# Performance work log

Measured on AMD Instinct MI355X. Metric: run time of the kernel, lower is better.

## Reference

```python
import jax, jax.numpy as jnp
from jax import lax
import numpy as np

B, S, H, DIN, BIN, NH, NL = 32, 256, 256, 16, 2, 8, 3
DH = H // NH


def setup_inputs() -> dict:
    key = jax.random.key(0)
    it = iter(jax.random.split(key, 40))
    def nrm(shape, s=0.05):
        return jax.random.normal(next(it), shape, jnp.float32) * s
    return {
        "parts": jax.random.normal(next(it), (B, S, DIN), jnp.float32),
        "bin_info": jax.random.normal(next(it), (B, BIN), jnp.float32),
        "target": jax.random.randint(next(it), (B, S), 0, S, dtype=jnp.int32),
        "pe_W1": nrm((H // 2, DIN)), "pe_b1": jnp.zeros((H // 2,), jnp.float32),
        "pe_W2": nrm((H // 2, H // 2)), "pe_b2": jnp.zeros((H // 2,), jnp.float32),
        "be_W1": nrm((H // 4, BIN)), "be_b1": jnp.zeros((H // 4,), jnp.float32),
        "be_W2": nrm((H // 4, H // 4)), "be_b2": jnp.zeros((H // 4,), jnp.float32),
        "pos_emb": nrm((S, H // 4)),
        "tr_Wqkv": nrm((NL, 3 * H, H)), "tr_bqkv": jnp.zeros((NL, 3 * H), jnp.float32),
        "tr_Wo": nrm((NL, H, H)), "tr_bo": jnp.zeros((NL, H), jnp.float32),
        "tr_ln1_g": jnp.ones((NL, H), jnp.float32), "tr_ln1_b": jnp.zeros((NL, H), jnp.float32),
        "tr_ff_W1": nrm((NL, 2 * H, H)), "tr_ff_b1": jnp.zeros((NL, 2 * H), jnp.float32),
        "tr_ff_W2": nrm((NL, H, 2 * H)), "tr_ff_b2": jnp.zeros((NL, H), jnp.float32),
        "tr_ln2_g": jnp.ones((NL, H), jnp.float32), "tr_ln2_b": jnp.zeros((NL, H), jnp.float32),
        "lstm_Wih": nrm((4 * H, H)), "lstm_Whh": nrm((4 * H, H)),
        "lstm_bih": jnp.zeros((4 * H,), jnp.float32), "lstm_bhh": jnp.zeros((4 * H,), jnp.float32),
        "ptr_W": nrm((H, H)), "ptr_b": jnp.zeros((H,), jnp.float32),
        "ptr_v": nrm((H,)),
    }


def _ln(x, g, b):
    m = x.mean(-1, keepdims=True)
    v = ((x - m) ** 2).mean(-1, keepdims=True)
    return (x - m) / jnp.sqrt(v + 1e-5) * g + b


def _forward(parts, bin_info, target, pe_W1, pe_b1, pe_W2, pe_b2,
             be_W1, be_b1, be_W2, be_b2, pos_emb,
             tr_Wqkv, tr_bqkv, tr_Wo, tr_bo, tr_ln1_g, tr_ln1_b,
             tr_ff_W1, tr_ff_b1, tr_ff_W2, tr_ff_b2, tr_ln2_g, tr_ln2_b,
             lstm_Wih, lstm_Whh, lstm_bih, lstm_bhh, ptr_W, ptr_b, ptr_v):
    # --- encode_inputs (dropout inactive in eval) ---
    p = jax.nn.relu(parts @ pe_W1.T + pe_b1) @ pe_W2.T + pe_b2            # [B,S,H/2]
    bb = jax.nn.relu(bin_info @ be_W1.T + be_b1) @ be_W2.T + be_b2        # [B,H/4]
    bb = jnp.broadcast_to(bb[:, None, :], (B, S, H // 4))
    pe = jnp.broadcast_to(pos_emb[None], (B, S, H // 4))
    x = jnp.concatenate([p, bb, pe], axis=-1)                             # [B,S,H]
    scale = 1.0 / np.sqrt(DH)
    for l in range(NL):  # post-norm TransformerEncoderLayer, relu FFN
        qkv = x @ tr_Wqkv[l].T + tr_bqkv[l]
        q, k, v = jnp.split(qkv, 3, axis=-1)
        q = q.reshape(B, S, NH, DH).transpose(0, 2, 1, 3)
        k = k.reshape(B, S, NH, DH).transpose(0, 2, 1, 3)
        v = v.reshape(B, S, NH, DH).transpose(0, 2, 1, 3)
        a = jax.nn.softmax(jnp.einsum('bhqd,bhkd->bhqk', q, k) * scale, axis=-1)
        o = jnp.einsum('bhqk,bhkd->bhqd', a, v).transpose(0, 2, 1, 3).reshape(B, S, H)
        x = _ln(x + o @ tr_Wo[l].T + tr_bo[l], tr_ln1_g[l], tr_ln1_b[l])
        ff = jax.nn.relu(x @ tr_ff_W1[l].T + tr_ff_b1[l]) @ tr_ff_W2[l].T + tr_ff_b2[l]
        x = _ln(x + ff, tr_ln2_g[l], tr_ln2_b[l])
    enc = x
    # Note: the original's inner MultiheadAttention calls never feed the
    # returned step_logits (part_logit is overwritten), so the faithful output is
    # logits[b,t,i] = v . tanh(ptr(h_t) + ptr(enc_i)), vectorized over i here.
    e_proj = enc @ ptr_W.T + ptr_b                                        # [B,S,H]
    bidx = jnp.arange(B)

    def step(carry, tgt_t):
        h, c, xin = carry
        g = xin @ lstm_Wih.T + lstm_bih + h @ lstm_Whh.T + lstm_bhh
        i, f, gg, o = jnp.split(g, 4, axis=-1)
        c = jax.nn.sigmoid(f) * c + jax.nn.sigmoid(i) * jnp.tanh(gg)
        h = jax.nn.sigmoid(o) * jnp.tanh(c)
        hp = h @ ptr_W.T + ptr_b                                          # [B,H]
        logits = jnp.tanh(hp[:, None, :] + e_proj) @ ptr_v                # [B,S]
        nxt = enc[bidx, tgt_t]                                            # teacher forcing
        return (h, c, nxt), logits

    z = jnp.zeros((B, H), jnp.float32)
    _, logits = lax.scan(step, (z, z, z), target.T)                       # [S,B,S]
    return logits.transpose(1, 0, 2)                                      # [B,S,S]


def reference(parts, bin_info, target, pe_W1, pe_b1, pe_W2, pe_b2,
              be_W1, be_b1, be_W2, be_b2, pos_emb,
              tr_Wqkv, tr_bqkv, tr_Wo, tr_bo, tr_ln1_g, tr_ln1_b,
              tr_ff_W1, tr_ff_b1, tr_ff_W2, tr_ff_b2, tr_ln2_g, tr_ln2_b,
              lstm_Wih, lstm_Whh, lstm_bih, lstm_bhh, ptr_W, ptr_b, ptr_v):
    return _forward(parts, bin_info, target, pe_W1, pe_b1, pe_W2, pe_b2,
                    be_W1, be_b1, be_W2, be_b2, pos_emb,
                    tr_Wqkv, tr_bqkv, tr_Wo, tr_bo, tr_ln1_g, tr_ln1_b,
                    tr_ff_W1, tr_ff_b1, tr_ff_W2, tr_ff_b2, tr_ln2_g, tr_ln2_b,
                    lstm_Wih, lstm_Whh, lstm_bih, lstm_bhh, ptr_W, ptr_b, ptr_v)
```

## Files before the change

kernel.cpp:

```cpp
#include <hip/hip_runtime.h>
#include <cstddef>

#define DEV __device__ __forceinline__

DEV float fexp2(float x) { return __builtin_amdgcn_exp2f(x); }
DEV float frcp(float x)  { return __builtin_amdgcn_rcpf(x); }
DEV float fsigm(float x) { return frcp(1.0f + fexp2(-1.44269504f * x)); }
DEV float ftanh_(float x){ return 1.0f - 2.0f * frcp(1.0f + fexp2(2.88539008f * x)); }

typedef _Float16 h2t __attribute__((ext_vector_type(2)));
typedef _Float16 v8h __attribute__((ext_vector_type(8)));
typedef float v4f __attribute__((ext_vector_type(4)));
union U32H2 { unsigned int u; h2t h; };
DEV h2t u2h(unsigned int u) { U32H2 x; x.u = u; return x.h; }

template <int BM, int BN, bool RELU, bool OUTF16>
__global__ __launch_bounds__(256) void hgemm_kernel(
    const _Float16* __restrict__ A, const _Float16* __restrict__ W,
    const float* __restrict__ bias1, const float* __restrict__ bias2,
    void* __restrict__ Cout, int M, int N, int K)
{
    constexpr int MT = BM / 32;
    constexpr int NT = BN / 32;
    constexpr int RA = BM / 64;
    constexpr int RB = BN / 64;
    __shared__ _Float16 As[BM * 32];
    __shared__ _Float16 Bs[BN * 32];

    const int tid = threadIdx.x;
    const int lane = tid & 63;
    const int lm = lane & 15, lq = lane >> 4;
    const int wrow = ((tid >> 6) & 1) * (BM / 2);
    const int wcol = (tid >> 7) * (BN / 2);
    const int m0 = blockIdx.x * BM, n0 = blockIdx.y * BN;
    const _Float16* Ab = A + (size_t)m0 * K;
    const _Float16* Wb = W + (size_t)n0 * K;

    v4f acc[MT][NT];
#pragma unroll
    for (int i = 0; i < MT; ++i)
#pragma unroll
        for (int j = 0; j < NT; ++j) acc[i][j] = (v4f){0.f, 0.f, 0.f, 0.f};

    const int rowS = tid >> 2, qS = tid & 3;

    uint4 ra[RA], rb[RB];
#pragma unroll
    for (int r = 0; r < RA; ++r)
        ra[r] = *(const uint4*)(Ab + (size_t)(rowS + 64 * r) * K + qS * 8);
#pragma unroll
    for (int r = 0; r < RB; ++r)
        rb[r] = *(const uint4*)(Wb + (size_t)(rowS + 64 * r) * K + qS * 8);

    for (int k0 = 0; k0 < K; k0 += 32) {
        __syncthreads();
#pragma unroll
        for (int r = 0; r < RA; ++r)
            *(uint4*)(As + (size_t)(tid + 256 * r) * 8) = ra[r];
#pragma unroll
        for (int r = 0; r < RB; ++r)
            *(uint4*)(Bs + (size_t)(tid + 256 * r) * 8) = rb[r];
        __syncthreads();
        int kn = k0 + 32;
        if (kn < K) {
#pragma unroll
            for (int r = 0; r < RA; ++r)
                ra[r] = *(const uint4*)(Ab + (size_t)(rowS + 64 * r) * K + kn + qS * 8);
#pragma unroll
            for (int r = 0; r < RB; ++r)
                rb[r] = *(const uint4*)(Wb + (size_t)(rowS + 64 * r) * K + kn + qS * 8);
        }
        v8h af[MT], bf[NT];
#pragma unroll
        for (int i = 0; i < MT; ++i)
            af[i] = *(const v8h*)(As + (size_t)(wrow + i * 16 + lm) * 32 + lq * 8);
#pragma unroll
        for (int j = 0; j < NT; ++j)
            bf[j] = *(const v8h*)(Bs + (size_t)(wcol + j * 16 + lm) * 32 + lq * 8);
#pragma unroll
        for (int i = 0; i < MT; ++i)
#pragma unroll
            for (int j = 0; j < NT; ++j)
                acc[i][j] = __builtin_amdgcn_mfma_f32_16x16x32_f16(
                    af[i], bf[j], acc[i][j], 0, 0, 0);
    }

#pragma unroll
    for (int j = 0; j < NT; ++j) {
        int col = n0 + wcol + j * 16 + lm;
        float bv = bias1[col];
        if (bias2) bv += bias2[col];
#pragma unroll
        for (int i = 0; i < MT; ++i) {
            int rbase = m0 + wrow + i * 16 + lq * 4;
#pragma unroll
            for (int rg = 0; rg < 4; ++rg) {
                float vv = acc[i][j][rg] + bv;
                if (RELU) vv = fmaxf(vv, 0.f);
                if (OUTF16)
                    ((_Float16*)Cout)[(size_t)(rbase + rg) * N + col] = (_Float16)vv;
                else
                    ((float*)Cout)[(size_t)(rbase + rg) * N + col] = vv;
            }
        }
    }
}

__global__ __launch_bounds__(256) void hgemm_gather_kernel(
    const _Float16* __restrict__ X16, const int* __restrict__ target,
    const _Float16* __restrict__ W, const float* __restrict__ bias1,
    _Float16* __restrict__ Cout, int N, int K)
{
    constexpr int BM = 64, BN = 128, MT = 2, NT = 4, RB = 2;
    __shared__ _Float16 As[BM * 32];
    __shared__ _Float16 Bs[BN * 32];

    const int tid = threadIdx.x;
    const int lane = tid & 63;
    const int lm = lane & 15, lq = lane >> 4;
    const int wrow = ((tid >> 6) & 1) * (BM / 2);
    const int wcol = (tid >> 7) * (BN / 2);
    const int m0 = blockIdx.x * BM, n0 = blockIdx.y * BN;
    const _Float16* Wb = W + (size_t)n0 * K;

    v4f acc[MT][NT];
#pragma unroll
    for (int i = 0; i < MT; ++i)
#pragma unroll
        for (int j = 0; j < NT; ++j) acc[i][j] = (v4f){0.f, 0.f, 0.f, 0.f};

    const int rowS = tid >> 2, qS = tid & 3;

    const int m = m0 + rowS;
    const int bb = m >> 8, tt = m & 255;
    const bool valid = (tt > 0);
    const _Float16* arow = X16;
    if (valid) {
        int src = target[bb * 256 + tt - 1];
        arow = X16 + ((size_t)(bb * 256 + src)) * 256;
    }

    uint4 ra, rb[RB];
    ra = valid ? *(const uint4*)(arow + qS * 8) : (uint4){0u, 0u, 0u, 0u};
#pragma unroll
    for (int r = 0; r < RB; ++r)
        rb[r] = *(const uint4*)(Wb + (size_t)(rowS + 64 * r) * K + qS * 8);

    for (int k0 = 0; k0 < K; k0 += 32) {
        __syncthreads();
        *(uint4*)(As + (size_t)tid * 8) = ra;
#pragma unroll
        for (int r = 0; r < RB; ++r)
            *(uint4*)(Bs + (size_t)(tid + 256 * r) * 8) = rb[r];
        __syncthreads();
        int kn = k0 + 32;
        if (kn < K) {
            ra = valid ? *(const uint4*)(arow + kn + qS * 8)
                       : (uint4){0u, 0u, 0u, 0u};
#pragma unroll
            for (int r = 0; r < RB; ++r)
                rb[r] = *(const uint4*)(Wb + (size_t)(rowS + 64 * r) * K + kn + qS * 8);
        }
        v8h af[MT], bf[NT];
#pragma unroll
        for (int i = 0; i < MT; ++i)
            af[i] = *(const v8h*)(As + (size_t)(wrow + i * 16 + lm) * 32 + lq * 8);
#pragma unroll
        for (int j = 0; j < NT; ++j)
            bf[j] = *(const v8h*)(Bs + (size_t)(wcol + j * 16 + lm) * 32 + lq * 8);
#pragma unroll
        for (int i = 0; i < MT; ++i)
#pragma unroll
            for (int j = 0; j < NT; ++j)
                acc[i][j] = __builtin_amdgcn_mfma_f32_16x16x32_f16(
                    af[i], bf[j], acc[i][j], 0, 0, 0);
    }

#pragma unroll
    for (int j = 0; j < NT; ++j) {
        int col = n0 + wcol + j * 16 + lm;
        float bv = bias1[col];
#pragma unroll
        for (int i = 0; i < MT; ++i) {
            int rbase = m0 + wrow + i * 16 + lq * 4;
#pragma unroll
            for (int rg = 0; rg < 4; ++rg)
                Cout[(size_t)(rbase + rg) * N + col] =
                    (_Float16)(acc[i][j][rg] + bv);
        }
    }
}

__global__ __launch_bounds__(256) void hgemm_ln_kernel(
    const _Float16* __restrict__ A, const _Float16* __restrict__ W,
    const float* __restrict__ bias, const float* __restrict__ gamma,
    const float* __restrict__ beta, float* __restrict__ X,
    _Float16* __restrict__ X16, int K)
{
    constexpr int BM = 64, BN = 256, MT = 2, NT = 8, RA = 1, RB = 4;
    __shared__ _Float16 As[BM * 32];
    __shared__ _Float16 Bs[BN * 32];
    __shared__ float redS[2][BM][2];

    const int tid = threadIdx.x;
    const int lane = tid & 63;
    const int lm = lane & 15, lq = lane >> 4;
    const int wrow = ((tid >> 6) & 1) * 32;
    const int wcol = (tid >> 7) * 128;
    const int half = tid >> 7;
    const int m0 = blockIdx.x * BM;
    const _Float16* Ab = A + (size_t)m0 * K;

    v4f acc[MT][NT];
#pragma unroll
    for (int i = 0; i < MT; ++i)
#pragma unroll
        for (int j = 0; j < NT; ++j) acc[i][j] = (v4f){0.f, 0.f, 0.f, 0.f};

    const int rowS = tid >> 2, qS = tid & 3;

    uint4 ra[RA], rb[RB];
#pragma unroll
    for (int r = 0; r < RA; ++r)
        ra[r] = *(const uint4*)(Ab + (size_t)(rowS + 64 * r) * K + qS * 8);
#pragma unroll
    for (int r = 0; r < RB; ++r)
        rb[r] = *(const uint4*)(W + (size_t)(rowS + 64 * r) * K + qS * 8);

    for (int k0 = 0; k0 < K; k0 += 32) {
        __syncthreads();
#pragma unroll
        for (int r = 0; r < RA; ++r)
            *(uint4*)(As + (size_t)(tid + 256 * r) * 8) = ra[r];
#pragma unroll
        for (int r = 0; r < RB; ++r)
            *(uint4*)(Bs + (size_t)(tid + 256 * r) * 8) = rb[r];
        __syncthreads();
        int kn = k0 + 32;
        if (kn < K) {
#pragma unroll
            for (int r = 0; r < RA; ++r)
                ra[r] = *(const uint4*)(Ab + (size_t)(rowS + 64 * r) * K + kn + qS * 8);
#pragma unroll
            for (int r = 0; r < RB; ++r)
                rb[r] = *(const uint4*)(W + (size_t)(rowS + 64 * r) * K + kn + qS * 8);
        }
        v8h af[MT], bf[NT];
#pragma unroll
        for (int i = 0; i < MT; ++i)
            af[i] = *(const v8h*)(As + (size_t)(wrow + i * 16 + lm) * 32 + lq * 8);
#pragma unroll
        for (int j = 0; j < NT; ++j)
            bf[j] = *(const v8h*)(Bs + (size_t)(wcol + j * 16 + lm) * 32 + lq * 8);
#pragma unroll
        for (int i = 0; i < MT; ++i)
#pragma unroll
            for (int j = 0; j < NT; ++j)
                acc[i][j] = __builtin_amdgcn_mfma_f32_16x16x32_f16(
                    af[i], bf[j], acc[i][j], 0, 0, 0);
    }

    float s[MT][4], s2[MT][4];
#pragma unroll
    for (int i = 0; i < MT; ++i)
#pragma unroll
        for (int rg = 0; rg < 4; ++rg) { s[i][rg] = 0.f; s2[i][rg] = 0.f; }
#pragma unroll
    for (int j = 0; j < NT; ++j) {
        int col = wcol + j * 16 + lm;
        float bv = bias[col];
#pragma unroll
        for (int i = 0; i < MT; ++i) {
            int rbase = m0 + wrow + i * 16 + lq * 4;
#pragma unroll
            for (int rg = 0; rg < 4; ++rg) {
                float y = acc[i][j][rg] + bv + X[(size_t)(rbase + rg) * 256 + col];
                acc[i][j][rg] = y;
                s[i][rg] += y;
                s2[i][rg] += y * y;
            }
        }
    }
#pragma unroll
    for (int i = 0; i < MT; ++i)
#pragma unroll
        for (int rg = 0; rg < 4; ++rg) {
            float a = s[i][rg], b2 = s2[i][rg];
#pragma unroll
            for (int m = 1; m < 16; m <<= 1) {
                a += __shfl_xor(a, m);
                b2 += __shfl_xor(b2, m);
            }
            if (lm == 0) {
                int rloc = wrow + i * 16 + lq * 4 + rg;
                redS[half][rloc][0] = a;
                redS[half][rloc][1] = b2;
            }
        }
    __syncthreads();
#pragma unroll
    for (int i = 0; i < MT; ++i) {
#pragma unroll
        for (int rg = 0; rg < 4; ++rg) {
            int rloc = wrow + i * 16 + lq * 4 + rg;
            float st = redS[0][rloc][0] + redS[1][rloc][0];
            float s2t = redS[0][rloc][1] + redS[1][rloc][1];
            float mean = st * (1.f / 256.f);
            float var = s2t * (1.f / 256.f) - mean * mean;
            float inv = rsqrtf(var + 1e-5f);
            size_t rowb = (size_t)(m0 + rloc) * 256;
#pragma unroll
            for (int j = 0; j < NT; ++j) {
                int col = wcol + j * 16 + lm;
                float o = (acc[i][j][rg] - mean) * inv * gamma[col] + beta[col];
                X[rowb + col] = o;
                X16[rowb + col] = (_Float16)o;
            }
        }
    }
}

__global__ __launch_bounds__(256) void cvt_fused_kernel(
    const float* __restrict__ s0, const float* __restrict__ s1,
    const float* __restrict__ s2, const float* __restrict__ s3,
    const float* __restrict__ s4, const float* __restrict__ s5,
    _Float16* __restrict__ dst,
    const float* __restrict__ Whh, unsigned int* __restrict__ WB,
    const float* __restrict__ bih, const float* __restrict__ bhh,
    float* __restrict__ PB)
{
    if (blockIdx.x < 7424) {
        int i = blockIdx.x * 256 + threadIdx.x;
        if (i >= 1900544) return;
        float val;
        if (i < 589824)       val = s0[i];
        else if (i < 786432)  val = s1[i - 589824];
        else if (i < 1179648) val = s2[i - 786432];
        else if (i < 1572864) val = s3[i - 1179648];
        else if (i < 1835008) {
            int idx = i - 1572864;
            int rp = idx >> 8, k = idx & 255;
            int j = rp >> 2, g = rp & 3;
            val = s4[(g * 256 + j) * 256 + k];
        }
        else                  val = s5[i - 1835008];
        dst[i] = (_Float16)val;
    } else {
        int idx = (blockIdx.x - 7424) * 256 + threadIdx.x;
        if (idx < 1024) {
            int j = idx >> 2, g = idx & 3;
            PB[idx] = bih[g * 256 + j] + bhh[g * 256 + j];
        }
        int l = idx & 3;
        int gt = idx >> 2;
        int tid = gt & 511;
        int q = gt >> 9;
        int i, c;
        if (q < 8)       { i = q >> 1; c = q & 1; }
        else if (q < 52) { int qq = q - 8; i = qq / 11; c = 2 + qq % 11; }
        else             { int qq = q - 52; c = 13 + (qq >> 2); i = qq & 3; }
        int r = ((tid & 255) << 2) + i;
        int k = ((tid >> 8) << 7) + (c << 3) + (l << 1);
        _Float16 lo = (_Float16)Whh[r * 256 + k];
        _Float16 hi = (_Float16)Whh[r * 256 + k + 1];
        U32H2 x; x.h = h2t{lo, hi};
        WB[idx] = x.u;
    }
}

__global__ __launch_bounds__(128) void part_enc_kernel(
    const float* __restrict__ parts, const float* __restrict__ W1,
    const float* __restrict__ b1, const float* __restrict__ W2,
    const float* __restrict__ b2, const float* __restrict__ bin_info,
    const float* __restrict__ be_W1, const float* __restrict__ be_b1,
    const float* __restrict__ be_W2, const float* __restrict__ be_b2,
    const float* __restrict__ pos_emb, float* __restrict__ X,
    _Float16* __restrict__ X16)
{
    __shared__ float W2s[128][129];
    __shared__ float h1[128];
    __shared__ float pin[16];
    __shared__ float h1b[64];
    __shared__ float bb_s[64];
    int tid = threadIdx.x;
    int b = blockIdx.x >> 3, s0 = (blockIdx.x & 7) * 32;
    for (int l = 0; l < 128; ++l) W2s[l][tid] = W2[l * 128 + tid];
    {
        float x0 = bin_info[b * 2], x1 = bin_info[b * 2 + 1];
        if (tid < 64)
            h1b[tid] = fmaxf(be_W1[tid * 2] * x0 + be_W1[tid * 2 + 1] * x1
                             + be_b1[tid], 0.f);
        __syncthreads();
        if (tid < 64) {
            float a = be_b2[tid];
#pragma unroll 4
            for (int e = 0; e < 64; ++e) a += be_W2[tid * 64 + e] * h1b[e];
            bb_s[tid] = a;
        }
        __syncthreads();
    }
    float w1r[16];
#pragma unroll
    for (int k = 0; k < 16; ++k) w1r[k] = W1[tid * 16 + k];
    float bias1v = b1[tid], bias2v = b2[tid];
    for (int si = 0; si < 32; ++si) {
        int s = s0 + si;
        size_t row = (size_t)b * 256 + s;
        if (tid < 16) pin[tid] = parts[row * 16 + tid];
        __syncthreads();
        float h = bias1v;
#pragma unroll
        for (int k = 0; k < 16; ++k) h += w1r[k] * pin[k];
        h1[tid] = fmaxf(h, 0.f);
        __syncthreads();
        float acc = bias2v;
#pragma unroll 4
        for (int e = 0; e < 128; ++e) acc += W2s[tid][e] * h1[e];
        X[row * 256 + tid] = acc;
        X16[row * 256 + tid] = (_Float16)acc;
        if (tid < 64) {
            float bbv = bb_s[tid];
            float pev = pos_emb[s * 64 + tid];
            X[row * 256 + 128 + tid] = bbv;
            X[row * 256 + 192 + tid] = pev;
            X16[row * 256 + 128 + tid] = (_Float16)bbv;
            X16[row * 256 + 192 + tid] = (_Float16)pev;
        }
        __syncthreads();
    }
}

__global__ __launch_bounds__(256) void attn_mfma_kernel(
    const _Float16* __restrict__ QKV, _Float16* __restrict__ O16)
{
    int bh = blockIdx.x;
    int b = bh >> 3, h = bh & 7;
    const int tid = threadIdx.x;
    const int w = tid >> 6;
    const int lane = tid & 63;
    const int lm = lane & 15, lq = lane >> 4;
    const float c_se = 0.17677669529663687f * 1.44269504f;

    __shared__ _Float16 Ks[4][256][8];
    __shared__ _Float16 Vt[32][264];
    __shared__ _Float16 Ps[4][16][264];

    const _Float16* qkvb = QKV + (size_t)(b * 256) * 768 + h * 32;
    {
        int s = tid;
        const _Float16* kr = qkvb + (size_t)s * 768 + 256;
#pragma unroll
        for (int c = 0; c < 4; ++c)
            *(uint4*)&Ks[c][s][0] = *(const uint4*)(kr + c * 8);
        const _Float16* vr = qkvb + (size_t)s * 768 + 512;
        _Float16 vtmp[32];
        *(uint4*)&vtmp[0]  = *(const uint4*)(vr);
        *(uint4*)&vtmp[8]  = *(const uint4*)(vr + 8);
        *(uint4*)&vtmp[16] = *(const uint4*)(vr + 16);
        *(uint4*)&vtmp[24] = *(const uint4*)(vr + 24);
#pragma unroll
        for (int d = 0; d < 32; ++d) Vt[d][s] = vtmp[d];
    }
    __syncthreads();

#pragma unroll 1
    for (int st = 0; st < 4; ++st) {
        int rt = w * 4 + st;
        v8h qf = *(const v8h*)(QKV + (size_t)(b * 256 + rt * 16 + lm) * 768
                               + h * 32 + lq * 8);
        v4f acc[16];
#pragma unroll
        for (int ct = 0; ct < 16; ++ct) {
            v8h kf = *(const v8h*)&Ks[lq][ct * 16 + lm][0];
            acc[ct] = __builtin_amdgcn_mfma_f32_16x16x32_f16(
                qf, kf, (v4f){0.f, 0.f, 0.f, 0.f}, 0, 0, 0);
        }
        float sminv[4];
#pragma unroll
        for (int r = 0; r < 4; ++r) {
            float m = acc[0][r];
#pragma unroll
            for (int ct = 1; ct < 16; ++ct) m = fmaxf(m, acc[ct][r]);
#pragma unroll
            for (int msk = 1; msk < 16; msk <<= 1)
                m = fmaxf(m, __shfl_xor(m, msk));
            float ssum = 0.f;
#pragma unroll
            for (int ct = 0; ct < 16; ++ct) {
                float e = fexp2((acc[ct][r] - m) * c_se);
                acc[ct][r] = e;
                ssum += e;
            }
#pragma unroll
            for (int msk = 1; msk < 16; msk <<= 1)
                ssum += __shfl_xor(ssum, msk);
            sminv[r] = frcp(ssum);
        }
#pragma unroll
        for (int ct = 0; ct < 16; ++ct)
#pragma unroll
            for (int r = 0; r < 4; ++r)
                Ps[w][lq * 4 + r][ct * 16 + lm] =
                    (_Float16)(acc[ct][r] * sminv[r]);
#pragma unroll
        for (int dt = 0; dt < 2; ++dt) {
            v4f o = (v4f){0.f, 0.f, 0.f, 0.f};
#pragma unroll
            for (int jc = 0; jc < 8; ++jc) {
                v8h pf = *(const v8h*)&Ps[w][lm][jc * 32 + lq * 8];
                v8h vf = *(const v8h*)&Vt[dt * 16 + lm][jc * 32 + lq * 8];
                o = __builtin_amdgcn_mfma_f32_16x16x32_f16(pf, vf, o, 0, 0, 0);
            }
#pragma unroll
            for (int r = 0; r < 4; ++r)
                O16[(size_t)(b * 256 + rt * 16 + lq * 4 + r) * 256
                    + h * 32 + dt * 16 + lm] = (_Float16)o[r];
        }
    }
}

__global__ __launch_bounds__(512) void lstm_kernel(
    const _Float16* __restrict__ g_in, const uint4* __restrict__ WB4,
    _Float16* __restrict__ HALL16)
{
    const int b = blockIdx.x;
    const int tid = threadIdx.x;
    const int kh = tid >> 8, j4 = tid & 255;

    __shared__ uint4 WL4[4096];
    __shared__ float gpart[2][1024];
    __shared__ uint4 h2v[32];
    unsigned int* h2_s = (unsigned int*)h2v;

#pragma unroll
    for (int g = 0; g < 8; ++g) WL4[g * 512 + tid] = WB4[g * 512 + tid];
    uint4 wr[44];
#pragma unroll
    for (int q = 0; q < 44; ++q) wr[q] = WB4[(8 + q) * 512 + tid];
    if (tid < 128) h2_s[tid] = 0u;

    const _Float16* ginb = g_in + (size_t)b * 256 * 1024;
    uint2 gi = make_uint2(0u, 0u);
    if (tid < 256) gi = *(const uint2*)(ginb + tid * 4);
    float c_state = 0.f;
    const uint4* SW4 = WB4 + 52 * 512;
    __syncthreads();

    for (int t = 0; t < 256; ++t) {
        uint4 sw[12];
#pragma unroll
        for (int q = 0; q < 4; ++q) sw[q] = SW4[q * 512 + tid];

        float acc[4] = {0.f, 0.f, 0.f, 0.f};
#pragma unroll
        for (int c = 0; c < 16; ++c) {
            if (c == 2) {
#pragma unroll
                for (int q = 4; q < 8; ++q) sw[q] = SW4[q * 512 + tid];
            }
            if (c == 6) {
#pragma unroll
                for (int q = 8; q < 12; ++q) sw[q] = SW4[q * 512 + tid];
            }
            uint4 h4 = h2v[(kh << 4) + c];
            h2t hx = u2h(h4.x), hy = u2h(h4.y), hz = u2h(h4.z), hw = u2h(h4.w);
#pragma unroll
            for (int i = 0; i < 4; ++i) {
                uint4 w = (c < 2)  ? WL4[((i << 1) + c) * 512 + tid]
                        : (c < 13) ? wr[i * 11 + (c - 2)]
                                   : sw[((c - 13) << 2) + i];
                acc[i] = __builtin_amdgcn_fdot2(u2h(w.x), hx, acc[i], false);
                acc[i] = __builtin_amdgcn_fdot2(u2h(w.y), hy, acc[i], false);
                acc[i] = __builtin_amdgcn_fdot2(u2h(w.z), hz, acc[i], false);
                acc[i] = __builtin_amdgcn_fdot2(u2h(w.w), hw, acc[i], false);
            }
        }
        *(float4*)&gpart[kh][j4 << 2] = make_float4(acc[0], acc[1], acc[2], acc[3]);
        __syncthreads();

        if (tid < 256) {
            int j = tid;
            h2t p0 = u2h(gi.x), p1 = u2h(gi.y);
            float ig = (float)p0.x + gpart[0][j]       + gpart[1][j];
            float fg = (float)p0.y + gpart[0][j + 256] + gpart[1][j + 256];
            float gg = (float)p1.x + gpart[0][j + 512] + gpart[1][j + 512];
            float og = (float)p1.y + gpart[0][j + 768] + gpart[1][j + 768];
            c_state = fsigm(fg) * c_state + fsigm(ig) * ftanh_(gg);
            float h = fsigm(og) * ftanh_(c_state);
            HALL16[((size_t)(b * 256 + t)) * 256 + j] = (_Float16)h;
            U32H2 hxp; hxp.h = h2t{(_Float16)h, (_Float16)0.f};
            unsigned int hu = hxp.u & 0xffffu;
            unsigned int other = (unsigned int)__shfl_xor((int)hu, 1);
            if ((j & 1) == 0) h2_s[j >> 1] = hu | (other << 16);
            int tn = (t < 255) ? (t + 1) : 255;
            gi = *(const uint2*)(ginb + (size_t)tn * 1024 + j * 4);
        }
        __syncthreads();
    }
}

__global__ __launch_bounds__(256) void pointer_kernel(
    const float* __restrict__ HP, const float* __restrict__ EP,
    const float* __restrict__ v, float* __restrict__ out)
{
    int b = blockIdx.z, tt = blockIdx.y, it = blockIdx.x;
    __shared__ float hp_s[16][260];
    __shared__ float ep_s[16][260];
    __shared__ float v_s[256];
    __shared__ float red[4];
    int tid = threadIdx.x;
    const float cs = 2.88539008f;
    const float* hpb = HP + ((size_t)b * 256 + tt * 16) * 256;
    const float* epb = EP + ((size_t)b * 256 + it * 16) * 256;
#pragma unroll
    for (int l = 0; l < 4; ++l) {
        int idx = tid + l * 256;
        int r = idx >> 6, c4 = idx & 63;
        float4 hv = *(const float4*)(hpb + r * 256 + c4 * 4);
        hv.x *= cs; hv.y *= cs; hv.z *= cs; hv.w *= cs;
        *(float4*)&hp_s[r][c4 * 4] = hv;
        float4 ev = *(const float4*)(epb + r * 256 + c4 * 4);
        ev.x *= cs; ev.y *= cs; ev.z *= cs; ev.w *= cs;
        *(float4*)&ep_s[r][c4 * 4] = ev;
    }
    float vv = v[tid];
    v_s[tid] = vv;
    float vp = vv;
#pragma unroll
    for (int m = 1; m < 64; m <<= 1) vp += __shfl_xor(vp, m);
    if ((tid & 63) == 0) red[tid >> 6] = vp;
    __syncthreads();
    float vsum = red[0] + red[1] + red[2] + red[3];
    int tl = tid >> 4, il = tid & 15;
    float acc = 0.f;
#pragma unroll 4
    for (int d = 0; d < 256; ++d) {
        float sval = hp_s[tl][d] + ep_s[il][d];
        float r = frcp(1.0f + fexp2(sval));
        acc = fmaf(v_s[d], r, acc);
    }
    out[((size_t)b * 256 + tt * 16 + tl) * 256 + it * 16 + il] =
        vsum - 2.0f * acc;
}

extern "C" void kernel_launch(void* const* d_in, const int* in_sizes, int n_in,
                              void* d_out, int out_size, void* d_ws, size_t ws_size,
                              hipStream_t stream)
{
    const float* parts    = (const float*)d_in[0];
    const float* bin_info = (const float*)d_in[1];
    const int*   target   = (const int*)d_in[2];
    const float* pe_W1 = (const float*)d_in[3];
    const float* pe_b1 = (const float*)d_in[4];
    const float* pe_W2 = (const float*)d_in[5];
    const float* pe_b2 = (const float*)d_in[6];
    const float* be_W1 = (const float*)d_in[7];
    const float* be_b1 = (const float*)d_in[8];
    const float* be_W2 = (const float*)d_in[9];
    const float* be_b2 = (const float*)d_in[10];
    const float* pos_emb = (const float*)d_in[11];
    const float* tr_Wqkv = (const float*)d_in[12];
    const float* tr_bqkv = (const float*)d_in[13];
    const float* tr_Wo   = (const float*)d_in[14];
    const float* tr_bo   = (const float*)d_in[15];
    const float* tr_ln1_g = (const float*)d_in[16];
    const float* tr_ln1_b = (const float*)d_in[17];
    const float* tr_ff_W1 = (const float*)d_in[18];
    const float* tr_ff_b1 = (const float*)d_in[19];
    const float* tr_ff_W2 = (const float*)d_in[20];
    const float* tr_ff_b2 = (const float*)d_in[21];
    const float* tr_ln2_g = (const float*)d_in[22];
    const float* tr_ln2_b = (const float*)d_in[23];
    const float* lstm_Wih = (const float*)d_in[24];
    const float* lstm_Whh = (const float*)d_in[25];
    const float* lstm_bih = (const float*)d_in[26];
    const float* lstm_bhh = (const float*)d_in[27];
    const float* ptr_W = (const float*)d_in[28];
    const float* ptr_b = (const float*)d_in[29];
    const float* ptr_v = (const float*)d_in[30];

    float* ws = (float*)d_ws;
    float* X     = ws;
    float* S1    = X + 2097152;
    float* CF32  = S1 + 8388608;
    float* EPROJ = CF32 + 2097152;
    float* X16f  = EPROJ + 2097152;
    float* S2f   = X16f + 1048576;
    float* W16f  = S2f + 1048576;
    float* WBf   = W16f + 1048576;
    float* BBuf  = WBf + 131072;
    float* PB    = BBuf + 2048;

    _Float16* X16    = (_Float16*)X16f;
    _Float16* S2h    = (_Float16*)S2f;
    _Float16* HALL16 = S2h;
    _Float16* S1h    = (_Float16*)S1;
    _Float16* W16    = (_Float16*)W16f;
    _Float16* Wqkv16 = W16;
    _Float16* Wo16   = Wqkv16 + 589824;
    _Float16* Wff116 = Wo16 + 196608;
    _Float16* Wff216 = Wff116 + 393216;
    _Float16* Wih16  = Wff216 + 393216;
    _Float16* WpW16  = Wih16 + 262144;

    cvt_fused_kernel<<<7936, 256, 0, stream>>>(
        tr_Wqkv, tr_Wo, tr_ff_W1, tr_ff_W2, lstm_Wih, ptr_W, W16,
        lstm_Whh, (unsigned int*)WBf, lstm_bih, lstm_bhh, PB);

    part_enc_kernel<<<256, 128, 0, stream>>>(parts, pe_W1, pe_b1, pe_W2, pe_b2,
                                             bin_info, be_W1, be_b1, be_W2, be_b2,
                                             pos_emb, X, X16);

    for (int l = 0; l < 3; ++l) {
        hgemm_kernel<64, 128, false, true><<<dim3(128, 6), 256, 0, stream>>>(
            X16, Wqkv16 + (size_t)l * 196608, tr_bqkv + l * 768, nullptr,
            S1h, 8192, 768, 256);
        attn_mfma_kernel<<<256, 256, 0, stream>>>(S1h, S2h);
        hgemm_ln_kernel<<<128, 256, 0, stream>>>(
            S2h, Wo16 + (size_t)l * 65536, tr_bo + l * 256,
            tr_ln1_g + l * 256, tr_ln1_b + l * 256, X, X16, 256);
        hgemm_kernel<64, 128, true, true><<<dim3(128, 4), 256, 0, stream>>>(
            X16, Wff116 + (size_t)l * 131072, tr_ff_b1 + l * 512, nullptr,
            S1h, 8192, 512, 256);
        hgemm_ln_kernel<<<128, 256, 0, stream>>>(
            S1h, Wff216 + (size_t)l * 131072, tr_ff_b2 + l * 256,
            tr_ln2_g + l * 256, tr_ln2_b + l * 256, X, X16, 512);
    }

    hgemm_kernel<64, 64, false, false><<<dim3(128, 4), 256, 0, stream>>>(
        X16, WpW16, ptr_b, nullptr, EPROJ, 8192, 256, 256);
    hgemm_gather_kernel<<<dim3(128, 8), 256, 0, stream>>>(
        X16, target, Wih16, PB, S1h, 1024, 256);
    lstm_kernel<<<32, 512, 0, stream>>>(S1h, (const uint4*)WBf, HALL16);
    hgemm_kernel<64, 64, false, false><<<dim3(128, 4), 256, 0, stream>>>(
        HALL16, WpW16, ptr_b, nullptr, CF32, 8192, 256, 256);
    pointer_kernel<<<dim3(16, 16, 32), 256, 0, stream>>>(CF32, EPROJ, ptr_v,
                                                         (float*)d_out);
}
```

Before: 1.115 ms.

## Fold encoder projection GEMM into LSTM launch to overlap with recurrence

The separate EPROJ GEMM launch is removed. Its work is now done by 256 extra blocks appended to the LSTM kernel grid, so it runs on otherwise idle CUs while the 32 serial LSTM blocks execute. The LSTM shared memory is moved into a single dynamic-style byte buffer that both roles share. The risk is that the GEMM blocks compete with the latency-critical LSTM blocks for CU scheduling, and that the larger shared allocation limits occupancy of the GEMM part.

```diff
diff --git a/kernel.cpp b/kernel.cpp
--- a/kernel.cpp
+++ b/kernel.cpp
@@ -519,18 +519,83 @@
     }
 }
 
-__global__ __launch_bounds__(512) void lstm_kernel(
+__global__ __launch_bounds__(512) void lstm_eproj_kernel(
     const _Float16* __restrict__ g_in, const uint4* __restrict__ WB4,
-    _Float16* __restrict__ HALL16)
+    _Float16* __restrict__ HALL16,
+    const _Float16* __restrict__ X16, const _Float16* __restrict__ WpW,
+    const float* __restrict__ ptr_b, float* __restrict__ EPROJ)
 {
+    __shared__ __align__(16) unsigned char smem[86016];
+    const int tid = threadIdx.x;
+
+    if (blockIdx.x >= 32) {
+        _Float16* As = (_Float16*)smem;
+        _Float16* Bs = (_Float16*)(smem + 8192);
+        const int gb = (int)blockIdx.x - 32;
+        const int m0 = (gb & 63) * 128, n0 = (gb >> 6) * 64;
+        const int lane = tid & 63;
+        const int lm = lane & 15, lq = lane >> 4;
+        const int wr = (tid >> 6) & 3, wc = tid >> 8;
+        const _Float16* Ab = X16 + (size_t)m0 * 256;
+        const _Float16* Wb = WpW + (size_t)n0 * 256;
+
+        v4f acc[2][2];
+#pragma unroll
+        for (int i = 0; i < 2; ++i)
+#pragma unroll
+            for (int j = 0; j < 2; ++j) acc[i][j] = (v4f){0.f, 0.f, 0.f, 0.f};
+
+        const int rowSA = tid >> 2, qA = tid & 3;
+        const int rowSB = tid >> 3, qB = tid & 7;
+        uint4 ra = *(const uint4*)(Ab + (size_t)rowSA * 256 + qA * 8);
+        uint2 rb = *(const uint2*)(Wb + (size_t)rowSB * 256 + qB * 4);
+
+        for (int k0 = 0; k0 < 256; k0 += 32) {
+            __syncthreads();
+            *(uint4*)(As + (size_t)rowSA * 32 + qA * 8) = ra;
+            *(uint2*)(Bs + (size_t)rowSB * 32 + qB * 4) = rb;
+            __syncthreads();
+            int kn = k0 + 32;
+            if (kn < 256) {
+                ra = *(const uint4*)(Ab + (size_t)rowSA * 256 + kn + qA * 8);
+                rb = *(const uint2*)(Wb + (size_t)rowSB * 256 + kn + qB * 4);
+            }
+            v8h af[2], bf[2];
+#pragma unroll
+            for (int i = 0; i < 2; ++i)
+                af[i] = *(const v8h*)(As + (size_t)(wr * 32 + i * 16 + lm) * 32 + lq * 8);
+#pragma unroll
+            for (int j = 0; j < 2; ++j)
+                bf[j] = *(const v8h*)(Bs + (size_t)(wc * 32 + j * 16 + lm) * 32 + lq * 8);
+#pragma unroll
+            for (int i = 0; i < 2; ++i)
+#pragma unroll
+                for (int j = 0; j < 2; ++j)
+                    acc[i][j] = __builtin_amdgcn_mfma_f32_16x16x32_f16(
+                        af[i], bf[j], acc[i][j], 0, 0, 0);
+        }
+#pragma unroll
+        for (int j = 0; j < 2; ++j) {
+            int col = n0 + wc * 32 + j * 16 + lm;
+            float bv = ptr_b[col];
+#pragma unroll
+            for (int i = 0; i < 2; ++i) {
+                int rbase = m0 + wr * 32 + i * 16 + lq * 4;
+#pragma unroll
+                for (int rg = 0; rg < 4; ++rg)
+                    EPROJ[(size_t)(rbase + rg) * 256 + col] = acc[i][j][rg] + bv;
+            }
+        }
+        return;
+    }
+
+    uint4* WL4 = (uint4*)smem;
+    float* gpart = (float*)(smem + 65536);
+    uint4* h2v = (uint4*)(smem + 65536 + 8192);
+    unsigned int* h2_s = (unsigned int*)h2v;
+
     const int b = blockIdx.x;
-    const int tid = threadIdx.x;
     const int kh = tid >> 8, j4 = tid & 255;
-
-    __shared__ uint4 WL4[4096];
-    __shared__ float gpart[2][1024];
-    __shared__ uint4 h2v[32];
-    unsigned int* h2_s = (unsigned int*)h2v;
 
 #pragma unroll
     for (int g = 0; g < 8; ++g) WL4[g * 512 + tid] = WB4[g * 512 + tid];
@@ -575,16 +640,17 @@
                 acc[i] = __builtin_amdgcn_fdot2(u2h(w.w), hw, acc[i], false);
             }
         }
-        *(float4*)&gpart[kh][j4 << 2] = make_float4(acc[0], acc[1], acc[2], acc[3]);
+        *(float4*)&gpart[kh * 1024 + (j4 << 2)] =
+            make_float4(acc[0], acc[1], acc[2], acc[3]);
         __syncthreads();
 
         if (tid < 256) {
             int j = tid;
             h2t p0 = u2h(gi.x), p1 = u2h(gi.y);
-            float ig = (float)p0.x + gpart[0][j]       + gpart[1][j];
-            float fg = (float)p0.y + gpart[0][j + 256] + gpart[1][j + 256];
-            float gg = (float)p1.x + gpart[0][j + 512] + gpart[1][j + 512];
-            float og = (float)p1.y + gpart[0][j + 768] + gpart[1][j + 768];
+            float ig = (float)p0.x + gpart[j]        + gpart[1024 + j];
+            float fg = (float)p0.y + gpart[j + 256]  + gpart[1024 + j + 256];
+            float gg = (float)p1.x + gpart[j + 512]  + gpart[1024 + j + 512];
+            float og = (float)p1.y + gpart[j + 768]  + gpart[1024 + j + 768];
             c_state = fsigm(fg) * c_state + fsigm(ig) * ftanh_(gg);
             float h = fsigm(og) * ftanh_(c_state);
             HALL16[((size_t)(b * 256 + t)) * 256 + j] = (_Float16)h;
@@ -727,11 +793,10 @@
             tr_ln2_g + l * 256, tr_ln2_b + l * 256, X, X16, 512);
     }
 
-    hgemm_kernel<64, 64, false, false><<<dim3(128, 4), 256, 0, stream>>>(
-        X16, WpW16, ptr_b, nullptr, EPROJ, 8192, 256, 256);
     hgemm_gather_kernel<<<dim3(128, 8), 256, 0, stream>>>(
         X16, target, Wih16, PB, S1h, 1024, 256);
-    lstm_kernel<<<32, 512, 0, stream>>>(S1h, (const uint4*)WBf, HALL16);
+    lstm_eproj_kernel<<<288, 512, 0, stream>>>(
+        S1h, (const uint4*)WBf, HALL16, X16, WpW16, ptr_b, EPROJ);
     hgemm_kernel<64, 64, false, false><<<dim3(128, 4), 256, 0, stream>>>(
         HALL16, WpW16, ptr_b, nullptr, CF32, 8192, 256, 256);
     pointer_kernel<<<dim3(16, 16, 32), 256, 0, stream>>>(CF32, EPROJ, ptr_v,
```

Measured after the change: 1.096 ms, median of 2. No clear change (-1.7%).
